# Performance work log

Hardware: AMD Instinct MI355X
Metric: run time of the kernel (lower is better)

Reference implementation:

```python
import jax, jax.numpy as jnp
import numpy as np

B, K, D, E, P = 256, 36, 2048, 1024, 5  # batch, regions, img_dim, embed_size, n_partial

def _xavier(key, fan_in, fan_out):
    r = np.sqrt(6.0) / np.sqrt(fan_in + fan_out)
    return jax.random.uniform(key, (fan_in, fan_out), minval=-r, maxval=r, dtype=jnp.float32)

def setup_inputs() -> dict:
    key = jax.random.key(0)
    ks = jax.random.split(key, 10)
    images = jax.random.normal(ks[0], (B, K, D), jnp.float32)
    bboxes = jax.random.uniform(ks[1], (B, K, 4), dtype=jnp.float32)
    img_range = jax.random.randint(ks[2], (B, K, K), 0, 2).astype(jnp.float32)
    z = lambda n: jnp.zeros((n,), jnp.float32)
    return dict(
        images=images, bboxes=bboxes, img_range=img_range,
        gate_w1=_xavier(ks[3], D + 5, D), gate_b1=z(D),
        gate_w2=_xavier(ks[4], D, 1), gate_b2=z(1),
        node_w1=_xavier(ks[5], D + 5, D), node_b1=z(D),
        node_w2=_xavier(ks[6], D, D), node_b2=z(D),
        map_w1=_xavier(ks[7], D, D), map_b1=z(D),
        map_w2=_xavier(ks[8], D, E), map_b2=z(E),
    )

def l2norm(x, eps=1e-8):
    return x / (jnp.sqrt(jnp.sum(x * x, axis=-1, keepdims=True)) + eps)

def reference(images, bboxes, img_range,
              gate_w1, gate_b1, gate_w2, gate_b2,
              node_w1, node_b1, node_w2, node_b2,
              map_w1, map_b1, map_w2, map_b2):
    # spatial info: bbox coords + area
    area = (bboxes[:, :, 2] - bboxes[:, :, 0]) * (bboxes[:, :, 3] - bboxes[:, :, 1])
    s_infos = jnp.concatenate([bboxes, area[:, :, None]], axis=2)  # (B,K,5)
    x = jnp.concatenate([images, s_infos * 0.1], axis=2)           # (B,K,D+5)

    gate = jnp.maximum(x @ gate_w1 + gate_b1, 0.0) @ gate_w2 + gate_b2  # (B,K,1)
    m = jax.nn.sigmoid(gate)[..., 0]                                     # (B,K)
    v = jnp.maximum(x @ node_w1 + node_b1, 0.0) @ node_w2 + node_b2      # (B,K,D)

    # top-P relation selection; fall back to self index when relation != 1
    effe_rels, topk_idx = jax.lax.top_k(img_range, P)                    # (B,K,P)
    idx_background = jnp.broadcast_to(jnp.arange(K)[None, :, None], (B, K, P))
    effe_ids = jnp.where(effe_rels == 1, topk_idx, idx_background)       # (B,K,P) int

    # per-batch gather of neighbor features/weights (no (B,K,K,D) repeat)
    v_gather = jax.vmap(lambda vb, ib: vb[ib])(v, effe_ids)              # (B,K,P,D)
    m_gather = jax.vmap(lambda mb, ib: mb[ib])(m, effe_ids)              # (B,K,P)

    out = jnp.einsum('bkp,bkpd->bkd', m_gather, v_gather)                # weighted sum
    out = l2norm(out)
    imgs = images + out
    img_emb = jnp.maximum(imgs @ map_w1 + map_b1, 0.0) @ map_w2 + map_b2  # (B,K,E)
    return l2norm(img_emb)
```

## Files before the change

kernel.cpp:

```cpp
#include <hip/hip_runtime.h>
#include <stdint.h>


typedef unsigned short ushort_t;
typedef unsigned int uint32;
typedef __bf16 bf16x8 __attribute__((ext_vector_type(8)));
typedef float f32x4 __attribute__((ext_vector_type(4)));

__device__ __forceinline__ ushort_t f2bf(float f) {
  uint32 u = __float_as_uint(f);
  u += 0x7fffu + ((u >> 16) & 1u);
  return (ushort_t)(u >> 16);
}
__device__ __forceinline__ float bflo(uint32 u) { return __uint_as_float(u << 16); }
__device__ __forceinline__ float bfhi(uint32 u) { return __uint_as_float(u & 0xffff0000u); }

__device__ __forceinline__ void gl_lds16(const void* g, void* l) {
  __builtin_amdgcn_global_load_lds(
      (__attribute__((address_space(1))) void*)(void*)g,
      (__attribute__((address_space(3))) void*)l, 16, 0, 0);
}

__device__ __forceinline__ float blk_sum(float v, float* sred) {
#pragma unroll
  for (int o = 32; o > 0; o >>= 1) v += __shfl_down(v, o, 64);
  const int w = threadIdx.x >> 6;
  if ((threadIdx.x & 63) == 0) sred[w] = v;
  __syncthreads();
  return sred[0] + sred[1] + sred[2] + sred[3];
}

__global__ __launch_bounds__(256) void transpose_bf16(
    const float* __restrict__ src, ushort_t* __restrict__ dst, int RK, int CN) {
  __shared__ float tile[32][33];
  const int bx = blockIdx.x;
  const int by = blockIdx.y;
  const int c = bx * 32 + threadIdx.x;
#pragma unroll
  for (int t = 0; t < 4; ++t) {
    int r = by * 32 + threadIdx.y + t * 8;
    tile[threadIdx.y + t * 8][threadIdx.x] = src[(size_t)r * CN + c];
  }
  __syncthreads();
  const int dc = by * 32 + threadIdx.x;
#pragma unroll
  for (int t = 0; t < 4; ++t) {
    int dr = bx * 32 + threadIdx.y + t * 8;
    dst[(size_t)dr * RK + dc] = f2bf(tile[threadIdx.x][threadIdx.y + t * 8]);
  }
}

__global__ __launch_bounds__(256) void cvt_bf16(const float* __restrict__ src,
                                                ushort_t* __restrict__ dst) {
  size_t i = ((size_t)blockIdx.x * 256 + threadIdx.x) * 8;
  float4 a = *(const float4*)(src + i);
  float4 b = *(const float4*)(src + i + 4);
  uint4 o;
  o.x = (uint32)f2bf(a.x) | ((uint32)f2bf(a.y) << 16);
  o.y = (uint32)f2bf(a.z) | ((uint32)f2bf(a.w) << 16);
  o.z = (uint32)f2bf(b.x) | ((uint32)f2bf(b.y) << 16);
  o.w = (uint32)f2bf(b.z) | ((uint32)f2bf(b.w) << 16);
  *(uint4*)(dst + i) = o;
}

__global__ __launch_bounds__(256) void gemm_bt(
    const ushort_t* __restrict__ A, int lda,
    const ushort_t* __restrict__ Bt, int K,
    void* __restrict__ outp, int ldo, int mode,
    const float* __restrict__ bias,
    const float* __restrict__ gw1, const float* __restrict__ nw1,
    const float* __restrict__ gb1, const float* __restrict__ nb1,
    const float* __restrict__ bboxes) {
  __shared__ ushort_t sA[128 * 32];
  __shared__ ushort_t sB[128 * 32];
  const int tid = threadIdx.x;
  const int w = tid >> 6, l = tid & 63;
  const int wm = (w >> 1) * 64, wn = (w & 1) * 64;
  const int lr = l >> 4, lc = l & 15;
  const int mBase = blockIdx.y * 128, cBase = blockIdx.x * 128;

  const int r0 = tid >> 2;
  const int c8 = (tid & 3) * 8;
  const ushort_t* gA = A + (size_t)(mBase + r0) * lda + c8;
  const ushort_t* gB = Bt + (size_t)(cBase + r0) * K + c8;
  const size_t sA64 = (size_t)64 * lda;
  const size_t sB64 = (size_t)64 * K;
  char* ldsA0 = (char*)sA + w * 1024;
  char* ldsA1 = (char*)sA + 4096 + w * 1024;
  char* ldsB0 = (char*)sB + w * 1024;
  char* ldsB1 = (char*)sB + 4096 + w * 1024;

  f32x4 acc[4][4] = {};

  for (int k0 = 0; k0 < K; k0 += 32) {
    gl_lds16(gA + k0, ldsA0);
    gl_lds16(gA + sA64 + k0, ldsA1);
    gl_lds16(gB + k0, ldsB0);
    gl_lds16(gB + sB64 + k0, ldsB1);
    __syncthreads();
    bf16x8 af[4], bfr[4];
#pragma unroll
    for (int i = 0; i < 4; ++i)
      af[i] = *(const bf16x8*)&sA[(wm + i * 16 + lc) * 32 + lr * 8];
#pragma unroll
    for (int j = 0; j < 4; ++j)
      bfr[j] = *(const bf16x8*)&sB[(wn + j * 16 + lc) * 32 + lr * 8];
#pragma unroll
    for (int i = 0; i < 4; ++i)
#pragma unroll
      for (int j = 0; j < 4; ++j)
        acc[i][j] = __builtin_amdgcn_mfma_f32_16x16x32_bf16(af[i], bfr[j], acc[i][j], 0, 0, 0);
    __syncthreads();
  }

  if (mode == 1) {
    const bool gate = (cBase < 2048);
    const float* b1 = gate ? gb1 : nb1;
    const float* wsrc = gate ? gw1 : nw1;
    const int coffs = gate ? 0 : 2048;
    float bcol[4], w5[4][5];
#pragma unroll
    for (int j = 0; j < 4; ++j) {
      int c = cBase + wn + j * 16 + lc - coffs;
      bcol[j] = b1[c];
#pragma unroll
      for (int t = 0; t < 5; ++t) w5[j][t] = wsrc[(size_t)(2048 + t) * 2048 + c];
    }
    ushort_t* O = (ushort_t*)outp;
#pragma unroll
    for (int i = 0; i < 4; ++i)
#pragma unroll
      for (int e = 0; e < 4; ++e) {
        size_t rg = mBase + wm + i * 16 + lr * 4 + e;
        const float* bb = bboxes + rg * 4;
        float s0 = bb[0], s1 = bb[1], s2 = bb[2], s3 = bb[3];
        float s4 = (s2 - s0) * (s3 - s1);
#pragma unroll
        for (int j = 0; j < 4; ++j) {
          float corr = 0.1f * (s0 * w5[j][0] + s1 * w5[j][1] + s2 * w5[j][2] +
                               s3 * w5[j][3] + s4 * w5[j][4]);
          float v = acc[i][j][e] + bcol[j] + corr;
          v = v > 0.f ? v : 0.f;
          O[rg * ldo + (cBase + wn + j * 16 + lc)] = f2bf(v);
        }
      }
  } else {
    float bcol[4];
#pragma unroll
    for (int j = 0; j < 4; ++j) bcol[j] = bias[cBase + wn + j * 16 + lc];
    if (mode == 4) {
      float* O = (float*)outp;
#pragma unroll
      for (int i = 0; i < 4; ++i)
#pragma unroll
        for (int e = 0; e < 4; ++e) {
          size_t rg = mBase + wm + i * 16 + lr * 4 + e;
#pragma unroll
          for (int j = 0; j < 4; ++j)
            O[rg * ldo + (cBase + wn + j * 16 + lc)] = acc[i][j][e] + bcol[j];
        }
    } else {
      const bool do_relu = (mode == 3);
      ushort_t* O = (ushort_t*)outp;
#pragma unroll
      for (int i = 0; i < 4; ++i)
#pragma unroll
        for (int e = 0; e < 4; ++e) {
          size_t rg = mBase + wm + i * 16 + lr * 4 + e;
#pragma unroll
          for (int j = 0; j < 4; ++j) {
            float v = acc[i][j][e] + bcol[j];
            if (do_relu && v < 0.f) v = 0.f;
            O[rg * ldo + (cBase + wn + j * 16 + lc)] = f2bf(v);
          }
        }
    }
  }
}

__global__ __launch_bounds__(256) void gate2_k(const ushort_t* __restrict__ hcat,
                                               const float* __restrict__ gw2,
                                               const float* __restrict__ gb2,
                                               float* __restrict__ msig) {
  __shared__ float sred[4];
  const int row = blockIdx.x;
  const int d0 = threadIdx.x * 8;
  uint4 u = *(const uint4*)(hcat + (size_t)row * 4096 + d0);
  float4 w0 = *(const float4*)(gw2 + d0);
  float4 w1 = *(const float4*)(gw2 + d0 + 4);
  float s = bflo(u.x) * w0.x + bfhi(u.x) * w0.y + bflo(u.y) * w0.z + bfhi(u.y) * w0.w +
            bflo(u.z) * w1.x + bfhi(u.z) * w1.y + bflo(u.w) * w1.z + bfhi(u.w) * w1.w;
  float tot = blk_sum(s, sred);
  if (threadIdx.x == 0) msig[row] = 1.f / (1.f + expf(-(tot + gb2[0])));
}

__global__ __launch_bounds__(256) void aggregate_k(const float* __restrict__ img_range,
                                                   const float* __restrict__ msig,
                                                   const ushort_t* __restrict__ vbf,
                                                   const float* __restrict__ images,
                                                   ushort_t* __restrict__ imgs_out) {
  __shared__ int s_id[5];
  __shared__ float s_w[5];
  __shared__ float sred[4];
  const int row = blockIdx.x;
  const int b = row / 36, k = row - b * 36;
  const int tid = threadIdx.x;
  if (tid < 64) {
    float val = (tid < 36) ? img_range[(size_t)row * 36 + tid] : 0.f;
    unsigned long long mask = __ballot(val == 1.0f);
    if (tid < 5) {
      unsigned long long mm = mask;
      for (int p = 0; p < tid; ++p) mm &= (mm - 1);
      int id = mm ? (int)__builtin_ctzll(mm) : k;
      s_id[tid] = id;
      s_w[tid] = msig[b * 36 + id];
    }
  }
  __syncthreads();
  const int d0 = tid * 8;
  float acc8[8] = {0, 0, 0, 0, 0, 0, 0, 0};
#pragma unroll
  for (int p = 0; p < 5; ++p) {
    uint4 u = *(const uint4*)(vbf + ((size_t)(b * 36 + s_id[p])) * 2048 + d0);
    float wg = s_w[p];
    acc8[0] += wg * bflo(u.x); acc8[1] += wg * bfhi(u.x);
    acc8[2] += wg * bflo(u.y); acc8[3] += wg * bfhi(u.y);
    acc8[4] += wg * bflo(u.z); acc8[5] += wg * bfhi(u.z);
    acc8[6] += wg * bflo(u.w); acc8[7] += wg * bfhi(u.w);
  }
  float ss = 0;
#pragma unroll
  for (int e = 0; e < 8; ++e) ss += acc8[e] * acc8[e];
  float tot = blk_sum(ss, sred);
  float inv = 1.f / (sqrtf(tot) + 1e-8f);
  const float* im = images + (size_t)row * 2048 + d0;
  float4 x0 = *(const float4*)im;
  float4 x1 = *(const float4*)(im + 4);
  float r[8] = {x0.x + acc8[0] * inv, x0.y + acc8[1] * inv, x0.z + acc8[2] * inv,
                x0.w + acc8[3] * inv, x1.x + acc8[4] * inv, x1.y + acc8[5] * inv,
                x1.z + acc8[6] * inv, x1.w + acc8[7] * inv};
  uint4 o;
  o.x = (uint32)f2bf(r[0]) | ((uint32)f2bf(r[1]) << 16);
  o.y = (uint32)f2bf(r[2]) | ((uint32)f2bf(r[3]) << 16);
  o.z = (uint32)f2bf(r[4]) | ((uint32)f2bf(r[5]) << 16);
  o.w = (uint32)f2bf(r[6]) | ((uint32)f2bf(r[7]) << 16);
  *(uint4*)(imgs_out + (size_t)row * 2048 + d0) = o;
}

__global__ __launch_bounds__(256) void l2norm_k(const float* __restrict__ emb,
                                                float* __restrict__ out) {
  __shared__ float sred[4];
  size_t base = (size_t)blockIdx.x * 1024 + threadIdx.x * 4;
  float4 x = *(const float4*)(emb + base);
  float tot = blk_sum(x.x * x.x + x.y * x.y + x.z * x.z + x.w * x.w, sred);
  float inv = 1.f / (sqrtf(tot) + 1e-8f);
  float4 o = {x.x * inv, x.y * inv, x.z * inv, x.w * inv};
  *(float4*)(out + base) = o;
}

extern "C" void kernel_launch(void* const* d_in, const int* in_sizes, int n_in,
                              void* d_out, int out_size, void* d_ws, size_t ws_size,
                              hipStream_t stream) {
  (void)in_sizes; (void)n_in; (void)out_size; (void)ws_size;
  const float* images    = (const float*)d_in[0];
  const float* bboxes    = (const float*)d_in[1];
  const float* img_range = (const float*)d_in[2];
  const float* gate_w1   = (const float*)d_in[3];
  const float* gate_b1   = (const float*)d_in[4];
  const float* gate_w2   = (const float*)d_in[5];
  const float* gate_b2   = (const float*)d_in[6];
  const float* node_w1   = (const float*)d_in[7];
  const float* node_b1   = (const float*)d_in[8];
  const float* node_w2   = (const float*)d_in[9];
  const float* node_b2   = (const float*)d_in[10];
  const float* map_w1    = (const float*)d_in[11];
  const float* map_b1    = (const float*)d_in[12];
  const float* map_w2    = (const float*)d_in[13];
  const float* map_b2    = (const float*)d_in[14];

  char* ws = (char*)d_ws;
  size_t off = 0;
  auto take = [&](size_t bytes) {
    char* p = ws + off;
    off += (bytes + 255) & ~(size_t)255;
    return p;
  };
  ushort_t* W1t  = (ushort_t*)take((size_t)4096 * 2048 * 2);
  ushort_t* W2t  = (ushort_t*)take((size_t)2048 * 2048 * 2);
  ushort_t* W3t  = (ushort_t*)take((size_t)2048 * 2048 * 2);
  ushort_t* W4t  = (ushort_t*)take((size_t)1024 * 2048 * 2);
  ushort_t* Abuf = (ushort_t*)take((size_t)9216 * 2048 * 2);
  ushort_t* Hcat = (ushort_t*)take((size_t)9216 * 4096 * 2);
  ushort_t* Vbuf = (ushort_t*)take((size_t)9216 * 2048 * 2);
  float*    Msig = (float*)take((size_t)9216 * 4);
  float*    Emb  = (float*)Hcat;

  dim3 tb(32, 8);
  transpose_bf16<<<dim3(64, 64), tb, 0, stream>>>(gate_w1, W1t, 2048, 2048);
  transpose_bf16<<<dim3(64, 64), tb, 0, stream>>>(node_w1, W1t + (size_t)2048 * 2048, 2048, 2048);
  transpose_bf16<<<dim3(64, 64), tb, 0, stream>>>(node_w2, W2t, 2048, 2048);
  transpose_bf16<<<dim3(64, 64), tb, 0, stream>>>(map_w1, W3t, 2048, 2048);
  transpose_bf16<<<dim3(32, 64), tb, 0, stream>>>(map_w2, W4t, 2048, 1024);
  cvt_bf16<<<9216, 256, 0, stream>>>(images, Abuf);

  gemm_bt<<<dim3(32, 72), 256, 0, stream>>>(Abuf, 2048, W1t, 2048, Hcat, 4096, 1,
                                            nullptr, gate_w1, node_w1, gate_b1, node_b1, bboxes);
  gate2_k<<<9216, 256, 0, stream>>>(Hcat, gate_w2, gate_b2, Msig);
  gemm_bt<<<dim3(16, 72), 256, 0, stream>>>(Hcat + 2048, 4096, W2t, 2048, Vbuf, 2048, 2,
                                            node_b2, nullptr, nullptr, nullptr, nullptr, nullptr);
  aggregate_k<<<9216, 256, 0, stream>>>(img_range, Msig, Vbuf, images, Abuf);
  gemm_bt<<<dim3(16, 72), 256, 0, stream>>>(Abuf, 2048, W3t, 2048, Vbuf, 2048, 3,
                                            map_b1, nullptr, nullptr, nullptr, nullptr, nullptr);
  gemm_bt<<<dim3(8, 72), 256, 0, stream>>>(Vbuf, 2048, W4t, 2048, Emb, 1024, 4,
                                           map_b2, nullptr, nullptr, nullptr, nullptr, nullptr);
  l2norm_k<<<9216, 256, 0, stream>>>(Emb, (float*)d_out);
}
```

Baseline: 893.6 us.

## Fuse gate second layer into first GEMM epilogue via atomic row sums

The gate half of the first GEMM no longer writes its ReLU hidden activations to memory. Each block multiplies them by gate_w2 in registers, reduces across lanes and atomically adds partial row sums into a zeroed buffer. The sigmoid moves into the aggregate kernel, which removes the separate gate2 kernel and roughly half of the hidden-buffer write and read traffic. The five weight-transpose launches are merged into one 3D-grid launch. In exchange it adds a memset, float atomics whose summation order is nondeterministic, and an extra shuffle reduction in the epilogue.

```diff
diff --git a/kernel.cpp b/kernel.cpp
--- a/kernel.cpp
+++ b/kernel.cpp
@@ -30,11 +30,25 @@
   return sred[0] + sred[1] + sred[2] + sred[3];
 }
 
-__global__ __launch_bounds__(256) void transpose_bf16(
-    const float* __restrict__ src, ushort_t* __restrict__ dst, int RK, int CN) {
+__global__ __launch_bounds__(256) void transpose_all(
+    const float* __restrict__ gw1, const float* __restrict__ nw1,
+    const float* __restrict__ nw2, const float* __restrict__ mw1,
+    const float* __restrict__ mw2,
+    ushort_t* __restrict__ W1t, ushort_t* __restrict__ W2t,
+    ushort_t* __restrict__ W3t, ushort_t* __restrict__ W4t) {
   __shared__ float tile[32][33];
-  const int bx = blockIdx.x;
-  const int by = blockIdx.y;
+  const float* src;
+  ushort_t* dst;
+  int CN = 2048;
+  switch (blockIdx.z) {
+    case 0: src = gw1; dst = W1t; break;
+    case 1: src = nw1; dst = W1t + (size_t)2048 * 2048; break;
+    case 2: src = nw2; dst = W2t; break;
+    case 3: src = mw1; dst = W3t; break;
+    default: src = mw2; dst = W4t; CN = 1024; break;
+  }
+  const int bx = blockIdx.x, by = blockIdx.y;
+  if (bx * 32 >= CN) return;
   const int c = bx * 32 + threadIdx.x;
 #pragma unroll
   for (int t = 0; t < 4; ++t) {
@@ -46,7 +60,7 @@
 #pragma unroll
   for (int t = 0; t < 4; ++t) {
     int dr = bx * 32 + threadIdx.y + t * 8;
-    dst[(size_t)dr * RK + dc] = f2bf(tile[threadIdx.x][threadIdx.y + t * 8]);
+    dst[(size_t)dr * 2048 + dc] = f2bf(tile[threadIdx.x][threadIdx.y + t * 8]);
   }
 }
 
@@ -70,7 +84,8 @@
     const float* __restrict__ bias,
     const float* __restrict__ gw1, const float* __restrict__ nw1,
     const float* __restrict__ gb1, const float* __restrict__ nb1,
-    const float* __restrict__ bboxes) {
+    const float* __restrict__ bboxes,
+    const float* __restrict__ gw2, float* __restrict__ msum) {
   __shared__ ushort_t sA[128 * 32];
   __shared__ ushort_t sB[128 * 32];
   const int tid = threadIdx.x;
@@ -115,35 +130,67 @@
 
   if (mode == 1) {
     const bool gate = (cBase < 2048);
+    const int coffs = gate ? 0 : 2048;
     const float* b1 = gate ? gb1 : nb1;
     const float* wsrc = gate ? gw1 : nw1;
-    const int coffs = gate ? 0 : 2048;
-    float bcol[4], w5[4][5];
+    float bcol[4], w5[4][5], g2c[4];
 #pragma unroll
     for (int j = 0; j < 4; ++j) {
       int c = cBase + wn + j * 16 + lc - coffs;
       bcol[j] = b1[c];
 #pragma unroll
       for (int t = 0; t < 5; ++t) w5[j][t] = wsrc[(size_t)(2048 + t) * 2048 + c];
+      g2c[j] = gate ? gw2[c] : 0.f;
     }
-    ushort_t* O = (ushort_t*)outp;
-#pragma unroll
-    for (int i = 0; i < 4; ++i)
-#pragma unroll
-      for (int e = 0; e < 4; ++e) {
-        size_t rg = mBase + wm + i * 16 + lr * 4 + e;
-        const float* bb = bboxes + rg * 4;
-        float s0 = bb[0], s1 = bb[1], s2 = bb[2], s3 = bb[3];
-        float s4 = (s2 - s0) * (s3 - s1);
-#pragma unroll
-        for (int j = 0; j < 4; ++j) {
-          float corr = 0.1f * (s0 * w5[j][0] + s1 * w5[j][1] + s2 * w5[j][2] +
-                               s3 * w5[j][3] + s4 * w5[j][4]);
-          float v = acc[i][j][e] + bcol[j] + corr;
-          v = v > 0.f ? v : 0.f;
-          O[rg * ldo + (cBase + wn + j * 16 + lc)] = f2bf(v);
+    if (gate) {
+      float rsum[4][4];
+#pragma unroll
+      for (int i = 0; i < 4; ++i)
+#pragma unroll
+        for (int e = 0; e < 4; ++e) {
+          size_t rg = mBase + wm + i * 16 + lr * 4 + e;
+          const float* bb = bboxes + rg * 4;
+          float s0 = bb[0], s1 = bb[1], s2 = bb[2], s3 = bb[3];
+          float s4 = (s2 - s0) * (s3 - s1);
+          float ar = 0.f;
+#pragma unroll
+          for (int j = 0; j < 4; ++j) {
+            float corr = 0.1f * (s0 * w5[j][0] + s1 * w5[j][1] + s2 * w5[j][2] +
+                                 s3 * w5[j][3] + s4 * w5[j][4]);
+            float v = acc[i][j][e] + bcol[j] + corr;
+            v = v > 0.f ? v : 0.f;
+            ar += v * g2c[j];
+          }
+          rsum[i][e] = ar;
         }
-      }
+#pragma unroll
+      for (int m = 1; m < 16; m <<= 1)
+#pragma unroll
+        for (int i = 0; i < 4; ++i)
+#pragma unroll
+          for (int e = 0; e < 4; ++e) rsum[i][e] += __shfl_xor(rsum[i][e], m, 64);
+      const int ii = lc >> 2, ee = lc & 3;
+      atomicAdd(&msum[mBase + wm + ii * 16 + lr * 4 + ee], rsum[ii][ee]);
+    } else {
+      ushort_t* O = (ushort_t*)outp;
+#pragma unroll
+      for (int i = 0; i < 4; ++i)
+#pragma unroll
+        for (int e = 0; e < 4; ++e) {
+          size_t rg = mBase + wm + i * 16 + lr * 4 + e;
+          const float* bb = bboxes + rg * 4;
+          float s0 = bb[0], s1 = bb[1], s2 = bb[2], s3 = bb[3];
+          float s4 = (s2 - s0) * (s3 - s1);
+#pragma unroll
+          for (int j = 0; j < 4; ++j) {
+            float corr = 0.1f * (s0 * w5[j][0] + s1 * w5[j][1] + s2 * w5[j][2] +
+                                 s3 * w5[j][3] + s4 * w5[j][4]);
+            float v = acc[i][j][e] + bcol[j] + corr;
+            v = v > 0.f ? v : 0.f;
+            O[rg * ldo + (cBase - 2048 + wn + j * 16 + lc)] = f2bf(v);
+          }
+        }
+    }
   } else {
     float bcol[4];
 #pragma unroll
@@ -178,24 +225,9 @@
   }
 }
 
-__global__ __launch_bounds__(256) void gate2_k(const ushort_t* __restrict__ hcat,
-                                               const float* __restrict__ gw2,
-                                               const float* __restrict__ gb2,
-                                               float* __restrict__ msig) {
-  __shared__ float sred[4];
-  const int row = blockIdx.x;
-  const int d0 = threadIdx.x * 8;
-  uint4 u = *(const uint4*)(hcat + (size_t)row * 4096 + d0);
-  float4 w0 = *(const float4*)(gw2 + d0);
-  float4 w1 = *(const float4*)(gw2 + d0 + 4);
-  float s = bflo(u.x) * w0.x + bfhi(u.x) * w0.y + bflo(u.y) * w0.z + bfhi(u.y) * w0.w +
-            bflo(u.z) * w1.x + bfhi(u.z) * w1.y + bflo(u.w) * w1.z + bfhi(u.w) * w1.w;
-  float tot = blk_sum(s, sred);
-  if (threadIdx.x == 0) msig[row] = 1.f / (1.f + expf(-(tot + gb2[0])));
-}
-
 __global__ __launch_bounds__(256) void aggregate_k(const float* __restrict__ img_range,
-                                                   const float* __restrict__ msig,
+                                                   const float* __restrict__ msum,
+                                                   const float* __restrict__ gb2,
                                                    const ushort_t* __restrict__ vbf,
                                                    const float* __restrict__ images,
                                                    ushort_t* __restrict__ imgs_out) {
@@ -213,7 +245,7 @@
       for (int p = 0; p < tid; ++p) mm &= (mm - 1);
       int id = mm ? (int)__builtin_ctzll(mm) : k;
       s_id[tid] = id;
-      s_w[tid] = msig[b * 36 + id];
+      s_w[tid] = 1.f / (1.f + expf(-(msum[b * 36 + id] + gb2[0])));
     }
   }
   __syncthreads();
@@ -290,28 +322,28 @@
   ushort_t* W3t  = (ushort_t*)take((size_t)2048 * 2048 * 2);
   ushort_t* W4t  = (ushort_t*)take((size_t)1024 * 2048 * 2);
   ushort_t* Abuf = (ushort_t*)take((size_t)9216 * 2048 * 2);
-  ushort_t* Hcat = (ushort_t*)take((size_t)9216 * 4096 * 2);
+  ushort_t* Hn   = (ushort_t*)take((size_t)9216 * 2048 * 2);
   ushort_t* Vbuf = (ushort_t*)take((size_t)9216 * 2048 * 2);
-  float*    Msig = (float*)take((size_t)9216 * 4);
-  float*    Emb  = (float*)Hcat;
-
-  dim3 tb(32, 8);
-  transpose_bf16<<<dim3(64, 64), tb, 0, stream>>>(gate_w1, W1t, 2048, 2048);
-  transpose_bf16<<<dim3(64, 64), tb, 0, stream>>>(node_w1, W1t + (size_t)2048 * 2048, 2048, 2048);
-  transpose_bf16<<<dim3(64, 64), tb, 0, stream>>>(node_w2, W2t, 2048, 2048);
-  transpose_bf16<<<dim3(64, 64), tb, 0, stream>>>(map_w1, W3t, 2048, 2048);
-  transpose_bf16<<<dim3(32, 64), tb, 0, stream>>>(map_w2, W4t, 2048, 1024);
+  float*    Msum = (float*)take((size_t)9216 * 4);
+  float*    Emb  = (float*)Vbuf;
+
+  hipMemsetAsync(Msum, 0, (size_t)9216 * 4, stream);
+  transpose_all<<<dim3(64, 64, 5), dim3(32, 8), 0, stream>>>(
+      gate_w1, node_w1, node_w2, map_w1, map_w2, W1t, W2t, W3t, W4t);
   cvt_bf16<<<9216, 256, 0, stream>>>(images, Abuf);
 
-  gemm_bt<<<dim3(32, 72), 256, 0, stream>>>(Abuf, 2048, W1t, 2048, Hcat, 4096, 1,
-                                            nullptr, gate_w1, node_w1, gate_b1, node_b1, bboxes);
-  gate2_k<<<9216, 256, 0, stream>>>(Hcat, gate_w2, gate_b2, Msig);
-  gemm_bt<<<dim3(16, 72), 256, 0, stream>>>(Hcat + 2048, 4096, W2t, 2048, Vbuf, 2048, 2,
-                                            node_b2, nullptr, nullptr, nullptr, nullptr, nullptr);
-  aggregate_k<<<9216, 256, 0, stream>>>(img_range, Msig, Vbuf, images, Abuf);
-  gemm_bt<<<dim3(16, 72), 256, 0, stream>>>(Abuf, 2048, W3t, 2048, Vbuf, 2048, 3,
-                                            map_b1, nullptr, nullptr, nullptr, nullptr, nullptr);
-  gemm_bt<<<dim3(8, 72), 256, 0, stream>>>(Vbuf, 2048, W4t, 2048, Emb, 1024, 4,
-                                           map_b2, nullptr, nullptr, nullptr, nullptr, nullptr);
+  gemm_bt<<<dim3(32, 72), 256, 0, stream>>>(Abuf, 2048, W1t, 2048, Hn, 2048, 1,
+                                            nullptr, gate_w1, node_w1, gate_b1, node_b1,
+                                            bboxes, gate_w2, Msum);
+  gemm_bt<<<dim3(16, 72), 256, 0, stream>>>(Hn, 2048, W2t, 2048, Vbuf, 2048, 2,
+                                            node_b2, nullptr, nullptr, nullptr, nullptr,
+                                            nullptr, nullptr, nullptr);
+  aggregate_k<<<9216, 256, 0, stream>>>(img_range, Msum, gate_b2, Vbuf, images, Abuf);
+  gemm_bt<<<dim3(16, 72), 256, 0, stream>>>(Abuf, 2048, W3t, 2048, Hn, 2048, 3,
+                                            map_b1, nullptr, nullptr, nullptr, nullptr,
+                                            nullptr, nullptr, nullptr);
+  gemm_bt<<<dim3(8, 72), 256, 0, stream>>>(Hn, 2048, W4t, 2048, Emb, 1024, 4,
+                                           map_b2, nullptr, nullptr, nullptr, nullptr,
+                                           nullptr, nullptr, nullptr);
   l2norm_k<<<9216, 256, 0, stream>>>(Emb, (float*)d_out);
 }
```

New measurement: 1.217 ms. 36.2% more time.

## Fold spatial features into padded GEMM K dim and merge weight transposes

Applied to the files above, without the earlier changes.

Appends the five scaled bbox/area features to the bf16 activation rows, padding K to 2080, and transposes the extra weight rows into padded W1t. The first GEMM then covers the spatial term through MFMA instead of a per-element fp32 correction in the epilogue. The five weight transposes become one launch, and the epilogue is templated on mode. The cost is about 1.5% more K work in GEMM1, and the spatial inputs and weight rows are now rounded to bf16 instead of kept in fp32.

```diff
diff --git a/kernel.cpp b/kernel.cpp
--- a/kernel.cpp
+++ b/kernel.cpp
@@ -30,47 +30,73 @@
   return sred[0] + sred[1] + sred[2] + sred[3];
 }
 
-__global__ __launch_bounds__(256) void transpose_bf16(
-    const float* __restrict__ src, ushort_t* __restrict__ dst, int RK, int CN) {
+__global__ __launch_bounds__(256) void transpose_all(
+    const float* __restrict__ gw1, const float* __restrict__ nw1,
+    const float* __restrict__ nw2, const float* __restrict__ mw1,
+    const float* __restrict__ mw2,
+    ushort_t* __restrict__ W1t, ushort_t* __restrict__ W2t,
+    ushort_t* __restrict__ W3t, ushort_t* __restrict__ W4t) {
   __shared__ float tile[32][33];
-  const int bx = blockIdx.x;
-  const int by = blockIdx.y;
+  const float* src;
+  ushort_t* dst;
+  int RKsrc, RKdst, CN;
+  switch (blockIdx.z) {
+    case 0: src = gw1; dst = W1t;                        RKsrc = 2053; RKdst = 2080; CN = 2048; break;
+    case 1: src = nw1; dst = W1t + (size_t)2048 * 2080;  RKsrc = 2053; RKdst = 2080; CN = 2048; break;
+    case 2: src = nw2; dst = W2t;                        RKsrc = 2048; RKdst = 2048; CN = 2048; break;
+    case 3: src = mw1; dst = W3t;                        RKsrc = 2048; RKdst = 2048; CN = 2048; break;
+    default: src = mw2; dst = W4t;                       RKsrc = 2048; RKdst = 2048; CN = 1024; break;
+  }
+  const int bx = blockIdx.x, by = blockIdx.y;
+  if (bx * 32 >= CN || by * 32 >= RKdst) return;
   const int c = bx * 32 + threadIdx.x;
 #pragma unroll
   for (int t = 0; t < 4; ++t) {
     int r = by * 32 + threadIdx.y + t * 8;
-    tile[threadIdx.y + t * 8][threadIdx.x] = src[(size_t)r * CN + c];
+    tile[threadIdx.y + t * 8][threadIdx.x] = (r < RKsrc) ? src[(size_t)r * CN + c] : 0.f;
   }
   __syncthreads();
   const int dc = by * 32 + threadIdx.x;
 #pragma unroll
   for (int t = 0; t < 4; ++t) {
     int dr = bx * 32 + threadIdx.y + t * 8;
-    dst[(size_t)dr * RK + dc] = f2bf(tile[threadIdx.x][threadIdx.y + t * 8]);
-  }
-}
-
-__global__ __launch_bounds__(256) void cvt_bf16(const float* __restrict__ src,
-                                                ushort_t* __restrict__ dst) {
-  size_t i = ((size_t)blockIdx.x * 256 + threadIdx.x) * 8;
-  float4 a = *(const float4*)(src + i);
-  float4 b = *(const float4*)(src + i + 4);
+    dst[(size_t)dr * RKdst + dc] = f2bf(tile[threadIdx.x][threadIdx.y + t * 8]);
+  }
+}
+
+__global__ __launch_bounds__(256) void build_A(const float* __restrict__ images,
+                                               const float* __restrict__ bboxes,
+                                               ushort_t* __restrict__ A) {
+  const int row = blockIdx.x, tid = threadIdx.x;
+  size_t i = (size_t)row * 2048 + tid * 8;
+  float4 a = *(const float4*)(images + i);
+  float4 b = *(const float4*)(images + i + 4);
   uint4 o;
   o.x = (uint32)f2bf(a.x) | ((uint32)f2bf(a.y) << 16);
   o.y = (uint32)f2bf(a.z) | ((uint32)f2bf(a.w) << 16);
   o.z = (uint32)f2bf(b.x) | ((uint32)f2bf(b.y) << 16);
   o.w = (uint32)f2bf(b.z) | ((uint32)f2bf(b.w) << 16);
-  *(uint4*)(dst + i) = o;
-}
-
+  *(uint4*)(A + (size_t)row * 2080 + tid * 8) = o;
+  if (tid < 4) {
+    uint4 s = {0, 0, 0, 0};
+    if (tid == 0) {
+      const float* bb = bboxes + (size_t)row * 4;
+      float s0 = bb[0], s1 = bb[1], s2 = bb[2], s3 = bb[3];
+      float s4 = (s2 - s0) * (s3 - s1);
+      s.x = (uint32)f2bf(0.1f * s0) | ((uint32)f2bf(0.1f * s1) << 16);
+      s.y = (uint32)f2bf(0.1f * s2) | ((uint32)f2bf(0.1f * s3) << 16);
+      s.z = (uint32)f2bf(0.1f * s4);
+    }
+    *(uint4*)(A + (size_t)row * 2080 + 2048 + tid * 8) = s;
+  }
+}
+
+template <int MODE>
 __global__ __launch_bounds__(256) void gemm_bt(
     const ushort_t* __restrict__ A, int lda,
     const ushort_t* __restrict__ Bt, int K,
-    void* __restrict__ outp, int ldo, int mode,
-    const float* __restrict__ bias,
-    const float* __restrict__ gw1, const float* __restrict__ nw1,
-    const float* __restrict__ gb1, const float* __restrict__ nb1,
-    const float* __restrict__ bboxes) {
+    void* __restrict__ outp, int ldo,
+    const float* __restrict__ bias, const float* __restrict__ bias2, int nsplit) {
   __shared__ ushort_t sA[128 * 32];
   __shared__ ushort_t sB[128 * 32];
   const int tid = threadIdx.x;
@@ -113,69 +139,25 @@
     __syncthreads();
   }
 
-  if (mode == 1) {
-    const bool gate = (cBase < 2048);
-    const float* b1 = gate ? gb1 : nb1;
-    const float* wsrc = gate ? gw1 : nw1;
-    const int coffs = gate ? 0 : 2048;
-    float bcol[4], w5[4][5];
-#pragma unroll
-    for (int j = 0; j < 4; ++j) {
-      int c = cBase + wn + j * 16 + lc - coffs;
-      bcol[j] = b1[c];
-#pragma unroll
-      for (int t = 0; t < 5; ++t) w5[j][t] = wsrc[(size_t)(2048 + t) * 2048 + c];
+  const float* bp = (cBase < nsplit) ? bias : bias2;
+  const int cof = (cBase < nsplit) ? 0 : nsplit;
+  float bcol[4];
+#pragma unroll
+  for (int j = 0; j < 4; ++j) bcol[j] = bp[cBase + wn + j * 16 + lc - cof];
+#pragma unroll
+  for (int i = 0; i < 4; ++i)
+#pragma unroll
+    for (int e = 0; e < 4; ++e) {
+      size_t rg = mBase + wm + i * 16 + lr * 4 + e;
+#pragma unroll
+      for (int j = 0; j < 4; ++j) {
+        float v = acc[i][j][e] + bcol[j];
+        if (MODE == 0 && v < 0.f) v = 0.f;
+        size_t oi = rg * ldo + (cBase + wn + j * 16 + lc);
+        if (MODE == 2) ((float*)outp)[oi] = v;
+        else ((ushort_t*)outp)[oi] = f2bf(v);
+      }
     }
-    ushort_t* O = (ushort_t*)outp;
-#pragma unroll
-    for (int i = 0; i < 4; ++i)
-#pragma unroll
-      for (int e = 0; e < 4; ++e) {
-        size_t rg = mBase + wm + i * 16 + lr * 4 + e;
-        const float* bb = bboxes + rg * 4;
-        float s0 = bb[0], s1 = bb[1], s2 = bb[2], s3 = bb[3];
-        float s4 = (s2 - s0) * (s3 - s1);
-#pragma unroll
-        for (int j = 0; j < 4; ++j) {
-          float corr = 0.1f * (s0 * w5[j][0] + s1 * w5[j][1] + s2 * w5[j][2] +
-                               s3 * w5[j][3] + s4 * w5[j][4]);
-          float v = acc[i][j][e] + bcol[j] + corr;
-          v = v > 0.f ? v : 0.f;
-          O[rg * ldo + (cBase + wn + j * 16 + lc)] = f2bf(v);
-        }
-      }
-  } else {
-    float bcol[4];
-#pragma unroll
-    for (int j = 0; j < 4; ++j) bcol[j] = bias[cBase + wn + j * 16 + lc];
-    if (mode == 4) {
-      float* O = (float*)outp;
-#pragma unroll
-      for (int i = 0; i < 4; ++i)
-#pragma unroll
-        for (int e = 0; e < 4; ++e) {
-          size_t rg = mBase + wm + i * 16 + lr * 4 + e;
-#pragma unroll
-          for (int j = 0; j < 4; ++j)
-            O[rg * ldo + (cBase + wn + j * 16 + lc)] = acc[i][j][e] + bcol[j];
-        }
-    } else {
-      const bool do_relu = (mode == 3);
-      ushort_t* O = (ushort_t*)outp;
-#pragma unroll
-      for (int i = 0; i < 4; ++i)
-#pragma unroll
-        for (int e = 0; e < 4; ++e) {
-          size_t rg = mBase + wm + i * 16 + lr * 4 + e;
-#pragma unroll
-          for (int j = 0; j < 4; ++j) {
-            float v = acc[i][j][e] + bcol[j];
-            if (do_relu && v < 0.f) v = 0.f;
-            O[rg * ldo + (cBase + wn + j * 16 + lc)] = f2bf(v);
-          }
-        }
-    }
-  }
 }
 
 __global__ __launch_bounds__(256) void gate2_k(const ushort_t* __restrict__ hcat,
@@ -285,33 +267,29 @@
     off += (bytes + 255) & ~(size_t)255;
     return p;
   };
-  ushort_t* W1t  = (ushort_t*)take((size_t)4096 * 2048 * 2);
+  ushort_t* W1t  = (ushort_t*)take((size_t)4096 * 2080 * 2);
   ushort_t* W2t  = (ushort_t*)take((size_t)2048 * 2048 * 2);
   ushort_t* W3t  = (ushort_t*)take((size_t)2048 * 2048 * 2);
   ushort_t* W4t  = (ushort_t*)take((size_t)1024 * 2048 * 2);
-  ushort_t* Abuf = (ushort_t*)take((size_t)9216 * 2048 * 2);
+  ushort_t* Abuf = (ushort_t*)take((size_t)9216 * 2080 * 2);
   ushort_t* Hcat = (ushort_t*)take((size_t)9216 * 4096 * 2);
   ushort_t* Vbuf = (ushort_t*)take((size_t)9216 * 2048 * 2);
   float*    Msig = (float*)take((size_t)9216 * 4);
-  float*    Emb  = (float*)Hcat;
-
-  dim3 tb(32, 8);
-  transpose_bf16<<<dim3(64, 64), tb, 0, stream>>>(gate_w1, W1t, 2048, 2048);
-  transpose_bf16<<<dim3(64, 64), tb, 0, stream>>>(node_w1, W1t + (size_t)2048 * 2048, 2048, 2048);
-  transpose_bf16<<<dim3(64, 64), tb, 0, stream>>>(node_w2, W2t, 2048, 2048);
-  transpose_bf16<<<dim3(64, 64), tb, 0, stream>>>(map_w1, W3t, 2048, 2048);
-  transpose_bf16<<<dim3(32, 64), tb, 0, stream>>>(map_w2, W4t, 2048, 1024);
-  cvt_bf16<<<9216, 256, 0, stream>>>(images, Abuf);
-
-  gemm_bt<<<dim3(32, 72), 256, 0, stream>>>(Abuf, 2048, W1t, 2048, Hcat, 4096, 1,
-                                            nullptr, gate_w1, node_w1, gate_b1, node_b1, bboxes);
+  float*    Emb  = (float*)Vbuf;
+
+  transpose_all<<<dim3(64, 65, 5), dim3(32, 8), 0, stream>>>(
+      gate_w1, node_w1, node_w2, map_w1, map_w2, W1t, W2t, W3t, W4t);
+  build_A<<<9216, 256, 0, stream>>>(images, bboxes, Abuf);
+
+  gemm_bt<0><<<dim3(32, 72), 256, 0, stream>>>(Abuf, 2080, W1t, 2080, Hcat, 4096,
+                                               gate_b1, node_b1, 2048);
   gate2_k<<<9216, 256, 0, stream>>>(Hcat, gate_w2, gate_b2, Msig);
-  gemm_bt<<<dim3(16, 72), 256, 0, stream>>>(Hcat + 2048, 4096, W2t, 2048, Vbuf, 2048, 2,
-                                            node_b2, nullptr, nullptr, nullptr, nullptr, nullptr);
+  gemm_bt<1><<<dim3(16, 72), 256, 0, stream>>>(Hcat + 2048, 4096, W2t, 2048, Vbuf, 2048,
+                                               node_b2, node_b2, 1 << 30);
   aggregate_k<<<9216, 256, 0, stream>>>(img_range, Msig, Vbuf, images, Abuf);
-  gemm_bt<<<dim3(16, 72), 256, 0, stream>>>(Abuf, 2048, W3t, 2048, Vbuf, 2048, 3,
-                                            map_b1, nullptr, nullptr, nullptr, nullptr, nullptr);
-  gemm_bt<<<dim3(8, 72), 256, 0, stream>>>(Vbuf, 2048, W4t, 2048, Emb, 1024, 4,
-                                           map_b2, nullptr, nullptr, nullptr, nullptr, nullptr);
+  gemm_bt<0><<<dim3(16, 72), 256, 0, stream>>>(Abuf, 2048, W3t, 2048, Hcat, 2048,
+                                               map_b1, map_b1, 1 << 30);
+  gemm_bt<2><<<dim3(8, 72), 256, 0, stream>>>(Hcat, 2048, W4t, 2048, Emb, 1024,
+                                              map_b2, map_b2, 1 << 30);
   l2norm_k<<<9216, 256, 0, stream>>>(Emb, (float*)d_out);
 }
```

New measurement: 744.8 us. 1.2x faster.
